# Kernel optimization log

Measured on AMD Instinct MI355X. Metric: run time of the kernel, lower is better.

The kernel has to match this reference:

```python
import jax, jax.numpy as jnp
import numpy as np

D_MODEL = 1024
HEADS = 16
D_K = D_MODEL // HEADS

def setup_inputs() -> dict:
    key = jax.random.key(0)
    ks = jax.random.split(key, 12)
    B, S = 4, 2048
    sc = 1.0 / np.sqrt(D_MODEL)
    inp = {
        'q': jax.random.normal(ks[0], (B, S, D_MODEL), jnp.float32),
        'k': jax.random.normal(ks[1], (B, S, D_MODEL), jnp.float32),
        'v': jax.random.normal(ks[2], (B, S, D_MODEL), jnp.float32),
        'mask': jnp.ones((B, S, S), jnp.int32),
        'Wq': jax.random.normal(ks[3], (D_MODEL, D_MODEL), jnp.float32) * sc,
        'bq': jnp.zeros((D_MODEL,), jnp.float32),
        'Wk': jax.random.normal(ks[4], (D_MODEL, D_MODEL), jnp.float32) * sc,
        'bk': jnp.zeros((D_MODEL,), jnp.float32),
        'Wv': jax.random.normal(ks[5], (D_MODEL, D_MODEL), jnp.float32) * sc,
        'bv': jnp.zeros((D_MODEL,), jnp.float32),
        'Wo': jax.random.normal(ks[6], (D_MODEL, D_MODEL), jnp.float32) * sc,
        'bo': jnp.zeros((D_MODEL,), jnp.float32),
    }
    return inp

def _proj_heads(x, W, b):
    # torch Linear: y = x @ W.T + b; then view(B,S,h,dk).transpose(1,2) -> [B,h,S,dk]
    B, S, _ = x.shape
    y = jnp.einsum('bsd,ed->bse', x, W) + b
    return y.reshape(B, S, HEADS, D_K).transpose(0, 2, 1, 3)

def reference(q, k, v, mask, Wq, bq, Wk, bk, Wv, bv, Wo, bo):
    B, S, _ = q.shape
    qh = _proj_heads(q, Wq, bq)  # [B,h,S,dk]
    kh = _proj_heads(k, Wk, bk)
    vh = _proj_heads(v, Wv, bv)
    scores = jnp.einsum('bhqd,bhkd->bhqk', qh, kh) / np.sqrt(D_K)
    scores = jnp.where(mask[:, None, :, :] == 0, jnp.float32(-1e9), scores)
    probs = jax.nn.softmax(scores, axis=-1)  # dropout = identity (eval mode)
    ctx = jnp.einsum('bhqk,bhkd->bhqd', probs, vh)
    concat = ctx.transpose(0, 2, 1, 3).reshape(B, S, D_MODEL)
    return jnp.einsum('bsd,ed->bse', concat, Wo) + bo
```

## Files before the change

kernel.cpp:

```cpp
#include <hip/hip_runtime.h>
#include <stdint.h>

#define DM 1024
#define SQL 2048
#define NB 4
#define NH 16
#define DK 64

typedef unsigned short u16;
typedef unsigned int u32;
typedef float f32x4 __attribute__((ext_vector_type(4)));
typedef short s16x8 __attribute__((ext_vector_type(8)));
typedef unsigned int u32x2 __attribute__((ext_vector_type(2)));

__device__ __forceinline__ u16 f2bf(float x) {
  union { float f; u32 u; } un; un.f = x;
  return (u16)((un.u + 0x8000u) >> 16);
}
__device__ __forceinline__ u32 pack_bf16(float a, float b) {
  union { float f; u32 u; } ua, ub; ua.f = a; ub.f = b;
  return ((ua.u + 0x8000u) >> 16) | ((ub.u + 0x8000u) & 0xFFFF0000u);
}

typedef __attribute__((address_space(3))) u32 lds_u32_t;
typedef __attribute__((address_space(1))) u32 g_u32_t;

__device__ __forceinline__ void async_cp16(void* lds, const void* g) {
  __builtin_amdgcn_global_load_lds((g_u32_t*)(unsigned long long)g,
                                   (lds_u32_t*)(unsigned long long)lds,
                                   16, 0, 0);
}

__device__ __forceinline__ void mfma16(f32x4& c, s16x8 a, s16x8 b) {
  c = __builtin_amdgcn_mfma_f32_16x16x32_bf16(a, b, c, 0, 0, 0);
}

__device__ __forceinline__ void xcd_tile_map(int flat, int& m0, int& n0) {
  const int xcd = flat & 7;
  const int j = flat >> 3;
  const int p = j >> 5;
  const int dm = (j >> 3) & 3;
  const int nn = j & 7;
  m0 = (p * 32 + xcd * 4 + dm) * 128;
  n0 = nn * 128;
}

__global__ void init_flag_k(int* flag) { if (threadIdx.x == 0) *flag = 1; }

__device__ __forceinline__ void store_bf4(u16* dst, float4 v) {
  u32 lo = pack_bf16(v.x, v.y);
  u32 hi = pack_bf16(v.z, v.w);
  ((u32*)dst)[0] = lo; ((u32*)dst)[1] = hi;
}

__global__ void __launch_bounds__(256) convert_scan_k(
    const float* __restrict__ q, const float* __restrict__ k, const float* __restrict__ v,
    const float* __restrict__ wq, const float* __restrict__ wk,
    const float* __restrict__ wv, const float* __restrict__ wo,
    const int* __restrict__ mask,
    u16* qb, u16* kb, u16* vb, u16* wqb, u16* wkb, u16* wvb, u16* wob, int* flag)
{
  const size_t i = (size_t)blockIdx.x * 256 + threadIdx.x;
  const size_t i4 = i * 4;
  store_bf4(qb + i4, *(const float4*)(q + i4));
  store_bf4(kb + i4, *(const float4*)(k + i4));
  store_bf4(vb + i4, *(const float4*)(v + i4));
  if (i4 < 1048576) {
    store_bf4(wqb + i4, *(const float4*)(wq + i4));
    store_bf4(wkb + i4, *(const float4*)(wk + i4));
    store_bf4(wvb + i4, *(const float4*)(wv + i4));
    store_bf4(wob + i4, *(const float4*)(wo + i4));
  }
  const size_t mi = i * 8;
  int4 m0 = *(const int4*)(mask + mi);
  int4 m1 = *(const int4*)(mask + mi + 4);
  bool z = (m0.x == 0) | (m0.y == 0) | (m0.z == 0) | (m0.w == 0) |
           (m1.x == 0) | (m1.y == 0) | (m1.z == 0) | (m1.w == 0);
  if (z) *flag = 0;
}

__device__ __forceinline__ void gemm_core(const u16* __restrict__ A, const u16* __restrict__ W,
                                          int m0, int n0, u16* sA, u16* sB, f32x4 (&acc)[4][4])
{
  const int tid = threadIdx.x;
  const int l = tid & 63, w = tid >> 6;
  const int g = l >> 4, ln = l & 15;
  const int wm = w & 1, wn = w >> 1;

  for (int kt = 0; kt < DM; kt += 64) {
#pragma unroll
    for (int i = 0; i < 4; ++i) {
      int s = w * 256 + i * 64 + l;
      int m = s >> 3;
      int kc = (s & 7) ^ (m & 7);
      async_cp16(sA + (size_t)(w * 256 + i * 64) * 8,
                 A + (size_t)(m0 + m) * DM + kt + kc * 8);
    }
#pragma unroll
    for (int i = 0; i < 4; ++i) {
      int s = w * 256 + i * 64 + l;
      int n = s >> 3;
      int kc = (s & 7) ^ (n & 7);
      async_cp16(sB + (size_t)(w * 256 + i * 64) * 8,
                 W + (size_t)(n0 + n) * DM + kt + kc * 8);
    }
    asm volatile("s_waitcnt vmcnt(0)" ::: "memory");
    __syncthreads();
#pragma unroll
    for (int ks = 0; ks < 2; ++ks) {
      s16x8 af[4], bfr[4];
#pragma unroll
      for (int mt = 0; mt < 4; ++mt) {
        int m = wm * 64 + mt * 16 + ln;
        int slot = m * 8 + ((ks * 4 + g) ^ (m & 7));
        af[mt] = *(const s16x8*)(sA + (size_t)slot * 8);
      }
#pragma unroll
      for (int nt = 0; nt < 4; ++nt) {
        int n = wn * 64 + nt * 16 + ln;
        int slot = n * 8 + ((ks * 4 + g) ^ (n & 7));
        bfr[nt] = *(const s16x8*)(sB + (size_t)slot * 8);
      }
#pragma unroll
      for (int mt = 0; mt < 4; ++mt)
#pragma unroll
        for (int nt = 0; nt < 4; ++nt)
          mfma16(acc[mt][nt], af[mt], bfr[nt]);
    }
    __syncthreads();
  }
}

__global__ void __launch_bounds__(256) gemm_qkv_k(
    const u16* __restrict__ qb, const u16* __restrict__ kb, const u16* __restrict__ vb,
    const u16* __restrict__ wqb, const u16* __restrict__ wkb, const u16* __restrict__ wvb,
    const float* __restrict__ bq, const float* __restrict__ bk, const float* __restrict__ bv,
    u16* Qh, u16* Kh, u16* Vt)
{
  __shared__ __align__(16) u16 sA[128 * 64];
  __shared__ __align__(16) u16 sB[128 * 64];
  const int z = blockIdx.z;
  const u16* A = (z == 0) ? qb : ((z == 1) ? kb : vb);
  const u16* W = (z == 0) ? wqb : ((z == 1) ? wkb : wvb);
  const float* bias = (z == 0) ? bq : ((z == 1) ? bk : bv);
  int m0, n0;
  xcd_tile_map(blockIdx.x + 8 * blockIdx.y, m0, n0);

  f32x4 zero4 = {0.f, 0.f, 0.f, 0.f};
  f32x4 acc[4][4];
#pragma unroll
  for (int mt = 0; mt < 4; ++mt)
#pragma unroll
    for (int nt = 0; nt < 4; ++nt) acc[mt][nt] = zero4;

  gemm_core(A, W, m0, n0, sA, sB, acc);

  const int tid = threadIdx.x;
  const int l = tid & 63, w = tid >> 6, g = l >> 4, ln = l & 15;
  const int wm = w & 1, wn = w >> 1;
  const float scale = (z == 0) ? (0.125f * 1.44269504089f) : 1.0f;
  u16* Crow = (z == 0) ? Qh : Kh;
#pragma unroll
  for (int nt = 0; nt < 4; ++nt) {
    int n = n0 + wn * 64 + nt * 16 + ln;
    float bn = bias[n];
#pragma unroll
    for (int mt = 0; mt < 4; ++mt) {
      int mb = m0 + wm * 64 + mt * 16 + g * 4;
      f32x4 vv = acc[mt][nt];
      if (z < 2) {
#pragma unroll
        for (int r = 0; r < 4; ++r)
          Crow[(size_t)(mb + r) * DM + n] = f2bf((vv[r] + bn) * scale);
      } else {
        int b = mb >> 11, s = mb & 2047;
        u32 lo = pack_bf16(vv[0] + bn, vv[1] + bn);
        u32 hi = pack_bf16(vv[2] + bn, vv[3] + bn);
        u32* dst = (u32*)(Vt + ((size_t)b << 21) + (size_t)n * SQL + s);
        dst[0] = lo; dst[1] = hi;
      }
    }
  }
}

__device__ __forceinline__ void p_transpose_frag(s16x8& out, u32 x0, u32 x1,
                                                 u32 y0, u32 y1,
                                                 int LA, int LB, bool ghi) {
  union { u32 wds[4]; s16x8 v; } pu;
#if __has_builtin(__builtin_amdgcn_permlane32_swap) && __has_builtin(__builtin_amdgcn_permlane16_swap)
  u32x2 r0 = __builtin_amdgcn_permlane32_swap(x0, y0, false, false);
  u32x2 s0 = __builtin_amdgcn_permlane16_swap(r0.x, r0.y, false, false);
  u32x2 r1 = __builtin_amdgcn_permlane32_swap(x1, y1, false, false);
  u32x2 s1 = __builtin_amdgcn_permlane16_swap(r1.x, r1.y, false, false);
  pu.wds[0] = s0.x; pu.wds[1] = s1.x; pu.wds[2] = s0.y; pu.wds[3] = s1.y;
#else
  u32 a0 = __shfl(x0, LA, 64), a1 = __shfl(x1, LA, 64);
  u32 b0 = __shfl(x0, LB, 64), b1 = __shfl(x1, LB, 64);
  u32 c0 = __shfl(y0, LA, 64), c1 = __shfl(y1, LA, 64);
  u32 d0 = __shfl(y0, LB, 64), d1 = __shfl(y1, LB, 64);
  pu.wds[0] = ghi ? c0 : a0;
  pu.wds[1] = ghi ? c1 : a1;
  pu.wds[2] = ghi ? d0 : b0;
  pu.wds[3] = ghi ? d1 : b1;
#endif
  out = pu.v;
}

__device__ __forceinline__ void attn_tile(
    const u16* Ks, const u16* Vs, int kv0,
    const s16x8 (&qf)[2][2], f32x4 (&ot)[4][2], f32x4 (&sums)[2],
    s16x8 ones, int allones, const int* __restrict__ mask,
    int b, int q0, int w, int g, int ln, int LA, int LB, bool ghi)
{
  f32x4 zero4 = {0.f, 0.f, 0.f, 0.f};
  __builtin_amdgcn_s_setprio(1);
#pragma unroll
  for (int kc = 0; kc < 2; ++kc) {
    f32x4 st[2][2];
#pragma unroll
    for (int t2 = 0; t2 < 2; ++t2)
#pragma unroll
      for (int u = 0; u < 2; ++u) st[t2][u] = zero4;
#pragma unroll
    for (int ks = 0; ks < 2; ++ks) {
#pragma unroll
      for (int t2 = 0; t2 < 2; ++t2) {
        int m = kc * 32 + t2 * 16 + ln;
        int slot = m * 8 + ((ks * 4 + g) ^ (m & 7));
        s16x8 kf = *(const s16x8*)(Ks + (size_t)slot * 8);
#pragma unroll
        for (int u = 0; u < 2; ++u) mfma16(st[t2][u], kf, qf[u][ks]);
      }
    }

    if (!allones) {
      const int* mb_ = mask + (size_t)b * SQL * SQL;
#pragma unroll
      for (int t2 = 0; t2 < 2; ++t2)
#pragma unroll
        for (int u = 0; u < 2; ++u)
#pragma unroll
          for (int r = 0; r < 4; ++r) {
            int kv = kv0 + kc * 32 + t2 * 16 + g * 4 + r;
            int qq = q0 + w * 32 + u * 16 + ln;
            if (mb_[(size_t)qq * SQL + kv] == 0) st[t2][u][r] = -30.f;
          }
    }

    s16x8 pf[2];
#pragma unroll
    for (int u = 0; u < 2; ++u) {
      u32 pkw[2][2];
#pragma unroll
      for (int t2 = 0; t2 < 2; ++t2) {
        float p0 = __builtin_amdgcn_exp2f(st[t2][u][0]);
        float p1 = __builtin_amdgcn_exp2f(st[t2][u][1]);
        float p2 = __builtin_amdgcn_exp2f(st[t2][u][2]);
        float p3 = __builtin_amdgcn_exp2f(st[t2][u][3]);
        pkw[t2][0] = pack_bf16(p0, p1);
        pkw[t2][1] = pack_bf16(p2, p3);
      }
      p_transpose_frag(pf[u], pkw[0][0], pkw[0][1], pkw[1][0], pkw[1][1], LA, LB, ghi);
      mfma16(sums[u], ones, pf[u]);
    }
#pragma unroll
    for (int mt = 0; mt < 4; ++mt) {
      int d = mt * 16 + ln;
      int slot = d * 8 + ((kc * 4 + g) ^ (d & 7));
      s16x8 vf = *(const s16x8*)(Vs + (size_t)slot * 8);
      mfma16(ot[mt][0], vf, pf[0]);
      mfma16(ot[mt][1], vf, pf[1]);
    }
  }
  __builtin_amdgcn_s_setprio(0);
}

__global__ void __launch_bounds__(256, 4) attn_k(
    const u16* __restrict__ Qh, const u16* __restrict__ Kh, const u16* __restrict__ Vt,
    const int* __restrict__ mask, const int* __restrict__ flag, u16* __restrict__ ctx)
{
  __shared__ __align__(16) u16 smem[17408];
  const int tid = threadIdx.x;
  const int l = tid & 63, w = tid >> 6, g = l >> 4, ln = l & 15;
  const int flat = blockIdx.x + 16 * (blockIdx.y + 16 * blockIdx.z);
  const int nid = (flat & 7) * 128 + (flat >> 3);
  const int q0 = (nid & 15) * 128;
  const int bh = nid >> 4;
  const int h = bh & 15, b = bh >> 4;
  const int allones = *flag;

  s16x8 qf[2][2];
#pragma unroll
  for (int u = 0; u < 2; ++u)
#pragma unroll
    for (int ks = 0; ks < 2; ++ks) {
      size_t row = (size_t)(b * SQL + q0 + w * 32 + u * 16 + ln);
      qf[u][ks] = *(const s16x8*)(Qh + row * DM + h * DK + ks * 32 + g * 8);
    }

  f32x4 zero4 = {0.f, 0.f, 0.f, 0.f};
  f32x4 ot[4][2];
#pragma unroll
  for (int mt = 0; mt < 4; ++mt)
#pragma unroll
    for (int u = 0; u < 2; ++u) ot[mt][u] = zero4;
  f32x4 sums[2];
  sums[0] = zero4; sums[1] = zero4;
  s16x8 ones;
#pragma unroll
  for (int i = 0; i < 8; ++i) ones[i] = (short)0x3F80;

  const int LA = (g & 1) * 32 + ln;
  const int LB = LA + 16;
  const bool ghi = (g >> 1) != 0;

  const int s0 = w * 128 + l, s1 = s0 + 64;
  const int m0r = s0 >> 3, m1r = s1 >> 3;
  const int c0 = ((s0 & 7) ^ (m0r & 7)) << 3;
  const int c1 = ((s1 & 7) ^ (m1r & 7)) << 3;
  const u16* gK0 = Kh + (size_t)(b * SQL + m0r) * DM + h * DK + c0;
  const u16* gK1 = Kh + (size_t)(b * SQL + m1r) * DM + h * DK + c1;
  const u16* gV0 = Vt + ((size_t)b << 21) + (size_t)(h * DK + m0r) * SQL + c0;
  const u16* gV1 = Vt + ((size_t)b << 21) + (size_t)(h * DK + m1r) * SQL + c1;
  u16* const dK = smem + (size_t)(w * 128) * 8;

#define STAGE_KV(BUFK, BUFV)                                           \
  do {                                                                 \
    async_cp16(dK + (BUFK), gK0);                                      \
    async_cp16(dK + (BUFK) + 512, gK1);                                \
    async_cp16(dK + (BUFV), gV0);                                      \
    async_cp16(dK + (BUFV) + 512, gV1);                                \
    gK0 += 64 * DM; gK1 += 64 * DM; gV0 += 64; gV1 += 64;              \
  } while (0)

  STAGE_KV(0, 4096);
  __syncthreads();

  for (int t = 0; t < 32; t += 2) {
    STAGE_KV(8192, 12288);
    attn_tile(smem, smem + 4096, t * 64, qf, ot, sums, ones, allones,
              mask, b, q0, w, g, ln, LA, LB, ghi);
    __syncthreads();
    if (t < 30) STAGE_KV(0, 4096);
    attn_tile(smem + 8192, smem + 12288, (t + 1) * 64, qf, ot, sums, ones,
              allones, mask, b, q0, w, g, ln, LA, LB, ghi);
    __syncthreads();
  }
#undef STAGE_KV

  float* red = (float*)smem;
#pragma unroll
  for (int u = 0; u < 2; ++u) {
    float inv = 1.0f / sums[u][0];
    int row = w * 32 + u * 16 + ln;
#pragma unroll
    for (int mt = 0; mt < 4; ++mt) {
      f32x4 vv = ot[mt][u] * inv;
      *(f32x4*)&red[(size_t)row * 68 + mt * 16 + g * 4] = vv;
    }
  }
  __syncthreads();
#pragma unroll
  for (int i = 0; i < 16; ++i) {
    int f2 = i * 256 + tid;
    int qq = f2 >> 5, dp = f2 & 31;
    float2 vv = *(const float2*)&red[(size_t)qq * 68 + dp * 2];
    u32 pkd = pack_bf16(vv.x, vv.y);
    *(u32*)(ctx + (size_t)(b * SQL + q0 + qq) * DM + h * DK + dp * 2) = pkd;
  }
}

__global__ void __launch_bounds__(256) gemm_out_k(
    const u16* __restrict__ ctx, const u16* __restrict__ wob,
    const float* __restrict__ bo, float* __restrict__ out)
{
  __shared__ __align__(16) u16 sA[128 * 64];
  __shared__ __align__(16) u16 sB[128 * 64];
  int m0, n0;
  xcd_tile_map(blockIdx.x + 8 * blockIdx.y, m0, n0);
  f32x4 zero4 = {0.f, 0.f, 0.f, 0.f};
  f32x4 acc[4][4];
#pragma unroll
  for (int mt = 0; mt < 4; ++mt)
#pragma unroll
    for (int nt = 0; nt < 4; ++nt) acc[mt][nt] = zero4;

  gemm_core(ctx, wob, m0, n0, sA, sB, acc);

  const int tid = threadIdx.x;
  const int l = tid & 63, w = tid >> 6, g = l >> 4, ln = l & 15;
  const int wm = w & 1, wn = w >> 1;
#pragma unroll
  for (int nt = 0; nt < 4; ++nt) {
    int n = n0 + wn * 64 + nt * 16 + ln;
    float bn = bo[n];
#pragma unroll
    for (int mt = 0; mt < 4; ++mt) {
      int mb = m0 + wm * 64 + mt * 16 + g * 4;
      f32x4 vv = acc[mt][nt];
#pragma unroll
      for (int r = 0; r < 4; ++r)
        out[(size_t)(mb + r) * DM + n] = vv[r] + bn;
    }
  }
}

extern "C" void kernel_launch(void* const* d_in, const int* in_sizes, int n_in,
                              void* d_out, int out_size, void* d_ws, size_t ws_size,
                              hipStream_t stream) {
  (void)in_sizes; (void)n_in; (void)out_size; (void)ws_size;
  const float* q  = (const float*)d_in[0];
  const float* k  = (const float*)d_in[1];
  const float* v  = (const float*)d_in[2];
  const int* mask = (const int*)d_in[3];
  const float* Wq = (const float*)d_in[4];
  const float* bq = (const float*)d_in[5];
  const float* Wk = (const float*)d_in[6];
  const float* bk = (const float*)d_in[7];
  const float* Wv = (const float*)d_in[8];
  const float* bv = (const float*)d_in[9];
  const float* Wo = (const float*)d_in[10];
  const float* bo = (const float*)d_in[11];
  float* out = (float*)d_out;
  char* ws = (char*)d_ws;

  u16* qb  = (u16*)(ws + 0);
  u16* kb  = (u16*)(ws + 16777216);
  u16* vb  = (u16*)(ws + 33554432);
  u16* Qh  = (u16*)(ws + 50331648);
  u16* Kh  = (u16*)(ws + 67108864);
  u16* Vt  = (u16*)(ws + 83886080);
  u16* ctx = (u16*)(ws + 100663296);
  u16* wqb = (u16*)(ws + 117440512);
  u16* wkb = (u16*)(ws + 119537664);
  u16* wvb = (u16*)(ws + 121634816);
  u16* wob = (u16*)(ws + 123731968);
  int* flag = (int*)(ws + 125829120);

  hipLaunchKernelGGL(init_flag_k, dim3(1), dim3(64), 0, stream, flag);
  hipLaunchKernelGGL(convert_scan_k, dim3(8192), dim3(256), 0, stream,
                     q, k, v, Wq, Wk, Wv, Wo, mask,
                     qb, kb, vb, wqb, wkb, wvb, wob, flag);
  hipLaunchKernelGGL(gemm_qkv_k, dim3(8, 64, 3), dim3(256), 0, stream,
                     qb, kb, vb, wqb, wkb, wvb, bq, bk, bv, Qh, Kh, Vt);
  hipLaunchKernelGGL(attn_k, dim3(16, 16, 4), dim3(256), 0, stream,
                     Qh, Kh, Vt, mask, flag, ctx);
  hipLaunchKernelGGL(gemm_out_k, dim3(8, 64), dim3(256), 0, stream,
                     ctx, wob, bo, out);
}
```

Measured before the change: 378.2 us.

## Shrink attention tiles to 64 queries and 32-key steps for higher occupancy

Each attention block now handles 64 query rows (16 per wave instead of 32), and each loop step stages 32 keys instead of 64. The grid doubles, LDS per block drops to 16 KB, and launch bounds request 8 blocks per CU. The epilogue stages bf16-packed values through LDS with a padded stride instead of fp32. The aim is more resident waves to hide latency, at the cost of loading each K/V tile for twice as many blocks and halving MFMA reuse of each K/V fragment.

```diff
diff --git a/kernel.cpp b/kernel.cpp
--- a/kernel.cpp
+++ b/kernel.cpp
@@ -206,106 +206,88 @@
   out = pu.v;
 }
 
-__device__ __forceinline__ void attn_tile(
+__device__ __forceinline__ void attn_tile32(
     const u16* Ks, const u16* Vs, int kv0,
-    const s16x8 (&qf)[2][2], f32x4 (&ot)[4][2], f32x4 (&sums)[2],
+    const s16x8 (&qf)[2], f32x4 (&ot)[4], f32x4& sums,
     s16x8 ones, int allones, const int* __restrict__ mask,
     int b, int q0, int w, int g, int ln, int LA, int LB, bool ghi)
 {
   f32x4 zero4 = {0.f, 0.f, 0.f, 0.f};
   __builtin_amdgcn_s_setprio(1);
-#pragma unroll
-  for (int kc = 0; kc < 2; ++kc) {
-    f32x4 st[2][2];
+  f32x4 st[2];
+  st[0] = zero4; st[1] = zero4;
+#pragma unroll
+  for (int ks = 0; ks < 2; ++ks) {
+#pragma unroll
+    for (int t2 = 0; t2 < 2; ++t2) {
+      int m = t2 * 16 + ln;
+      int slot = m * 8 + ((ks * 4 + g) ^ (m & 7));
+      s16x8 kf = *(const s16x8*)(Ks + (size_t)slot * 8);
+      mfma16(st[t2], kf, qf[ks]);
+    }
+  }
+
+  if (!allones) {
+    const int* mb_ = mask + (size_t)b * SQL * SQL;
 #pragma unroll
     for (int t2 = 0; t2 < 2; ++t2)
 #pragma unroll
-      for (int u = 0; u < 2; ++u) st[t2][u] = zero4;
-#pragma unroll
-    for (int ks = 0; ks < 2; ++ks) {
-#pragma unroll
-      for (int t2 = 0; t2 < 2; ++t2) {
-        int m = kc * 32 + t2 * 16 + ln;
-        int slot = m * 8 + ((ks * 4 + g) ^ (m & 7));
-        s16x8 kf = *(const s16x8*)(Ks + (size_t)slot * 8);
-#pragma unroll
-        for (int u = 0; u < 2; ++u) mfma16(st[t2][u], kf, qf[u][ks]);
+      for (int r = 0; r < 4; ++r) {
+        int kv = kv0 + t2 * 16 + g * 4 + r;
+        int qq = q0 + w * 16 + ln;
+        if (mb_[(size_t)qq * SQL + kv] == 0) st[t2][r] = -30.f;
       }
-    }
-
-    if (!allones) {
-      const int* mb_ = mask + (size_t)b * SQL * SQL;
-#pragma unroll
-      for (int t2 = 0; t2 < 2; ++t2)
-#pragma unroll
-        for (int u = 0; u < 2; ++u)
-#pragma unroll
-          for (int r = 0; r < 4; ++r) {
-            int kv = kv0 + kc * 32 + t2 * 16 + g * 4 + r;
-            int qq = q0 + w * 32 + u * 16 + ln;
-            if (mb_[(size_t)qq * SQL + kv] == 0) st[t2][u][r] = -30.f;
-          }
-    }
-
-    s16x8 pf[2];
-#pragma unroll
-    for (int u = 0; u < 2; ++u) {
-      u32 pkw[2][2];
-#pragma unroll
-      for (int t2 = 0; t2 < 2; ++t2) {
-        float p0 = __builtin_amdgcn_exp2f(st[t2][u][0]);
-        float p1 = __builtin_amdgcn_exp2f(st[t2][u][1]);
-        float p2 = __builtin_amdgcn_exp2f(st[t2][u][2]);
-        float p3 = __builtin_amdgcn_exp2f(st[t2][u][3]);
-        pkw[t2][0] = pack_bf16(p0, p1);
-        pkw[t2][1] = pack_bf16(p2, p3);
-      }
-      p_transpose_frag(pf[u], pkw[0][0], pkw[0][1], pkw[1][0], pkw[1][1], LA, LB, ghi);
-      mfma16(sums[u], ones, pf[u]);
-    }
-#pragma unroll
-    for (int mt = 0; mt < 4; ++mt) {
-      int d = mt * 16 + ln;
-      int slot = d * 8 + ((kc * 4 + g) ^ (d & 7));
-      s16x8 vf = *(const s16x8*)(Vs + (size_t)slot * 8);
-      mfma16(ot[mt][0], vf, pf[0]);
-      mfma16(ot[mt][1], vf, pf[1]);
-    }
+  }
+
+  u32 pkw[2][2];
+#pragma unroll
+  for (int t2 = 0; t2 < 2; ++t2) {
+    float p0 = __builtin_amdgcn_exp2f(st[t2][0]);
+    float p1 = __builtin_amdgcn_exp2f(st[t2][1]);
+    float p2 = __builtin_amdgcn_exp2f(st[t2][2]);
+    float p3 = __builtin_amdgcn_exp2f(st[t2][3]);
+    pkw[t2][0] = pack_bf16(p0, p1);
+    pkw[t2][1] = pack_bf16(p2, p3);
+  }
+  s16x8 pf;
+  p_transpose_frag(pf, pkw[0][0], pkw[0][1], pkw[1][0], pkw[1][1], LA, LB, ghi);
+  mfma16(sums, ones, pf);
+#pragma unroll
+  for (int mt = 0; mt < 4; ++mt) {
+    int d = mt * 16 + ln;
+    int slot = d * 4 + (g ^ ((d >> 1) & 3));
+    s16x8 vf = *(const s16x8*)(Vs + (size_t)slot * 8);
+    mfma16(ot[mt], vf, pf);
   }
   __builtin_amdgcn_s_setprio(0);
 }
 
-__global__ void __launch_bounds__(256, 4) attn_k(
+__global__ void __launch_bounds__(256, 8) attn_k(
     const u16* __restrict__ Qh, const u16* __restrict__ Kh, const u16* __restrict__ Vt,
     const int* __restrict__ mask, const int* __restrict__ flag, u16* __restrict__ ctx)
 {
-  __shared__ __align__(16) u16 smem[17408];
+  __shared__ __align__(16) u16 smem[8192];
   const int tid = threadIdx.x;
   const int l = tid & 63, w = tid >> 6, g = l >> 4, ln = l & 15;
-  const int flat = blockIdx.x + 16 * (blockIdx.y + 16 * blockIdx.z);
-  const int nid = (flat & 7) * 128 + (flat >> 3);
-  const int q0 = (nid & 15) * 128;
-  const int bh = nid >> 4;
+  const int flat = blockIdx.x + 32 * (blockIdx.y + 16 * blockIdx.z);
+  const int nid = (flat & 7) * 256 + (flat >> 3);
+  const int q0 = (nid & 31) * 64;
+  const int bh = nid >> 5;
   const int h = bh & 15, b = bh >> 4;
   const int allones = *flag;
 
-  s16x8 qf[2][2];
-#pragma unroll
-  for (int u = 0; u < 2; ++u)
-#pragma unroll
-    for (int ks = 0; ks < 2; ++ks) {
-      size_t row = (size_t)(b * SQL + q0 + w * 32 + u * 16 + ln);
-      qf[u][ks] = *(const s16x8*)(Qh + row * DM + h * DK + ks * 32 + g * 8);
-    }
+  s16x8 qf[2];
+#pragma unroll
+  for (int ks = 0; ks < 2; ++ks) {
+    size_t row = (size_t)(b * SQL + q0 + w * 16 + ln);
+    qf[ks] = *(const s16x8*)(Qh + row * DM + h * DK + ks * 32 + g * 8);
+  }
 
   f32x4 zero4 = {0.f, 0.f, 0.f, 0.f};
-  f32x4 ot[4][2];
-#pragma unroll
-  for (int mt = 0; mt < 4; ++mt)
-#pragma unroll
-    for (int u = 0; u < 2; ++u) ot[mt][u] = zero4;
-  f32x4 sums[2];
-  sums[0] = zero4; sums[1] = zero4;
+  f32x4 ot[4];
+#pragma unroll
+  for (int mt = 0; mt < 4; ++mt) ot[mt] = zero4;
+  f32x4 sums = zero4;
   s16x8 ones;
 #pragma unroll
   for (int i = 0; i < 8; ++i) ones[i] = (short)0x3F80;
@@ -314,59 +296,55 @@
   const int LB = LA + 16;
   const bool ghi = (g >> 1) != 0;
 
-  const int s0 = w * 128 + l, s1 = s0 + 64;
-  const int m0r = s0 >> 3, m1r = s1 >> 3;
-  const int c0 = ((s0 & 7) ^ (m0r & 7)) << 3;
-  const int c1 = ((s1 & 7) ^ (m1r & 7)) << 3;
-  const u16* gK0 = Kh + (size_t)(b * SQL + m0r) * DM + h * DK + c0;
-  const u16* gK1 = Kh + (size_t)(b * SQL + m1r) * DM + h * DK + c1;
-  const u16* gV0 = Vt + ((size_t)b << 21) + (size_t)(h * DK + m0r) * SQL + c0;
-  const u16* gV1 = Vt + ((size_t)b << 21) + (size_t)(h * DK + m1r) * SQL + c1;
-  u16* const dK = smem + (size_t)(w * 128) * 8;
+  const int mK = tid >> 3;
+  const int cK = ((tid & 7) ^ (mK & 7)) << 3;
+  const u16* gK = Kh + (size_t)(b * SQL + mK) * DM + h * DK + cK;
+  const int dV = tid >> 2;
+  const int cV = ((tid & 3) ^ ((dV >> 1) & 3)) << 3;
+  const u16* gV = Vt + ((size_t)b << 21) + (size_t)(h * DK + dV) * SQL + cV;
+  u16* const dst = smem + (size_t)w * 512;
 
 #define STAGE_KV(BUFK, BUFV)                                           \
   do {                                                                 \
-    async_cp16(dK + (BUFK), gK0);                                      \
-    async_cp16(dK + (BUFK) + 512, gK1);                                \
-    async_cp16(dK + (BUFV), gV0);                                      \
-    async_cp16(dK + (BUFV) + 512, gV1);                                \
-    gK0 += 64 * DM; gK1 += 64 * DM; gV0 += 64; gV1 += 64;              \
+    async_cp16(dst + (BUFK), gK);                                      \
+    async_cp16(dst + (BUFV), gV);                                      \
+    gK += 32 * DM; gV += 32;                                           \
   } while (0)
 
-  STAGE_KV(0, 4096);
+  STAGE_KV(0, 2048);
   __syncthreads();
 
-  for (int t = 0; t < 32; t += 2) {
-    STAGE_KV(8192, 12288);
-    attn_tile(smem, smem + 4096, t * 64, qf, ot, sums, ones, allones,
-              mask, b, q0, w, g, ln, LA, LB, ghi);
+  for (int t = 0; t < 64; t += 2) {
+    STAGE_KV(4096, 6144);
+    attn_tile32(smem, smem + 2048, t * 32, qf, ot, sums, ones, allones,
+                mask, b, q0, w, g, ln, LA, LB, ghi);
     __syncthreads();
-    if (t < 30) STAGE_KV(0, 4096);
-    attn_tile(smem + 8192, smem + 12288, (t + 1) * 64, qf, ot, sums, ones,
-              allones, mask, b, q0, w, g, ln, LA, LB, ghi);
+    if (t < 62) STAGE_KV(0, 2048);
+    attn_tile32(smem + 4096, smem + 6144, (t + 1) * 32, qf, ot, sums, ones,
+                allones, mask, b, q0, w, g, ln, LA, LB, ghi);
     __syncthreads();
   }
 #undef STAGE_KV
 
-  float* red = (float*)smem;
-#pragma unroll
-  for (int u = 0; u < 2; ++u) {
-    float inv = 1.0f / sums[u][0];
-    int row = w * 32 + u * 16 + ln;
+  u32* red = (u32*)smem;
+  {
+    float inv = 1.0f / sums[0];
+    int row = w * 16 + ln;
 #pragma unroll
     for (int mt = 0; mt < 4; ++mt) {
-      f32x4 vv = ot[mt][u] * inv;
-      *(f32x4*)&red[(size_t)row * 68 + mt * 16 + g * 4] = vv;
+      f32x4 vv = ot[mt] * inv;
+      int col = mt * 8 + g * 2;
+      red[(size_t)row * 33 + col]     = pack_bf16(vv[0], vv[1]);
+      red[(size_t)row * 33 + col + 1] = pack_bf16(vv[2], vv[3]);
     }
   }
   __syncthreads();
 #pragma unroll
-  for (int i = 0; i < 16; ++i) {
+  for (int i = 0; i < 8; ++i) {
     int f2 = i * 256 + tid;
     int qq = f2 >> 5, dp = f2 & 31;
-    float2 vv = *(const float2*)&red[(size_t)qq * 68 + dp * 2];
-    u32 pkd = pack_bf16(vv.x, vv.y);
-    *(u32*)(ctx + (size_t)(b * SQL + q0 + qq) * DM + h * DK + dp * 2) = pkd;
+    *(u32*)(ctx + (size_t)(b * SQL + q0 + qq) * DM + h * DK + dp * 2) =
+        red[(size_t)qq * 33 + dp];
   }
 }
 
@@ -443,7 +421,7 @@
                      qb, kb, vb, wqb, wkb, wvb, wob, flag);
   hipLaunchKernelGGL(gemm_qkv_k, dim3(8, 64, 3), dim3(256), 0, stream,
                      qb, kb, vb, wqb, wkb, wvb, bq, bk, bv, Qh, Kh, Vt);
-  hipLaunchKernelGGL(attn_k, dim3(16, 16, 4), dim3(256), 0, stream,
+  hipLaunchKernelGGL(attn_k, dim3(32, 16, 4), dim3(256), 0, stream,
                      Qh, Kh, Vt, mask, flag, ctx);
   hipLaunchKernelGGL(gemm_out_k, dim3(8, 64), dim3(256), 0, stream,
                      ctx, wob, bo, out);
```

After: 400.8 us. 1.06x slower.

## Double-buffer LDS tiles in projection GEMMs to overlap loads with MFMA

Applied to the files above, without the earlier changes.

Splits the GEMM main loop into separate stage (async global-to-LDS copy) and compute helpers. The next K-tile now loads into a second LDS buffer while the current tile is computed, aiming to hide global memory latency behind the MFMA work in the QKV and output projection kernels. It removes the explicit vmcnt wait and relies on the barrier to order the async copies. LDS use per block doubles, which may lower occupancy.

```diff
diff --git a/kernel.cpp b/kernel.cpp
--- a/kernel.cpp
+++ b/kernel.cpp
@@ -79,54 +79,73 @@
   if (z) *flag = 0;
 }
 
-__device__ __forceinline__ void gemm_core(const u16* __restrict__ A, const u16* __restrict__ W,
-                                          int m0, int n0, u16* sA, u16* sB, f32x4 (&acc)[4][4])
+__device__ __forceinline__ void gemm_stage(const u16* __restrict__ A,
+                                           const u16* __restrict__ W,
+                                           int m0, int n0, int kt,
+                                           u16* sA, u16* sB, int w, int l) {
+#pragma unroll
+  for (int i = 0; i < 4; ++i) {
+    int s = w * 256 + i * 64 + l;
+    int m = s >> 3;
+    int kc = (s & 7) ^ (m & 7);
+    async_cp16(sA + (size_t)(w * 256 + i * 64) * 8,
+               A + (size_t)(m0 + m) * DM + kt + kc * 8);
+  }
+#pragma unroll
+  for (int i = 0; i < 4; ++i) {
+    int s = w * 256 + i * 64 + l;
+    int n = s >> 3;
+    int kc = (s & 7) ^ (n & 7);
+    async_cp16(sB + (size_t)(w * 256 + i * 64) * 8,
+               W + (size_t)(n0 + n) * DM + kt + kc * 8);
+  }
+}
+
+__device__ __forceinline__ void gemm_compute(const u16* sA, const u16* sB,
+                                             f32x4 (&acc)[4][4],
+                                             int wm, int wn, int g, int ln) {
+#pragma unroll
+  for (int ks = 0; ks < 2; ++ks) {
+    s16x8 af[4], bfr[4];
+#pragma unroll
+    for (int mt = 0; mt < 4; ++mt) {
+      int m = wm * 64 + mt * 16 + ln;
+      int slot = m * 8 + ((ks * 4 + g) ^ (m & 7));
+      af[mt] = *(const s16x8*)(sA + (size_t)slot * 8);
+    }
+#pragma unroll
+    for (int nt = 0; nt < 4; ++nt) {
+      int n = wn * 64 + nt * 16 + ln;
+      int slot = n * 8 + ((ks * 4 + g) ^ (n & 7));
+      bfr[nt] = *(const s16x8*)(sB + (size_t)slot * 8);
+    }
+#pragma unroll
+    for (int mt = 0; mt < 4; ++mt)
+#pragma unroll
+      for (int nt = 0; nt < 4; ++nt)
+        mfma16(acc[mt][nt], af[mt], bfr[nt]);
+  }
+}
+
+__device__ __forceinline__ void gemm_core(const u16* __restrict__ A,
+                                          const u16* __restrict__ W,
+                                          int m0, int n0,
+                                          u16* sA0, u16* sB0, u16* sA1, u16* sB1,
+                                          f32x4 (&acc)[4][4])
 {
   const int tid = threadIdx.x;
   const int l = tid & 63, w = tid >> 6;
   const int g = l >> 4, ln = l & 15;
   const int wm = w & 1, wn = w >> 1;
 
-  for (int kt = 0; kt < DM; kt += 64) {
-#pragma unroll
-    for (int i = 0; i < 4; ++i) {
-      int s = w * 256 + i * 64 + l;
-      int m = s >> 3;
-      int kc = (s & 7) ^ (m & 7);
-      async_cp16(sA + (size_t)(w * 256 + i * 64) * 8,
-                 A + (size_t)(m0 + m) * DM + kt + kc * 8);
-    }
-#pragma unroll
-    for (int i = 0; i < 4; ++i) {
-      int s = w * 256 + i * 64 + l;
-      int n = s >> 3;
-      int kc = (s & 7) ^ (n & 7);
-      async_cp16(sB + (size_t)(w * 256 + i * 64) * 8,
-                 W + (size_t)(n0 + n) * DM + kt + kc * 8);
-    }
-    asm volatile("s_waitcnt vmcnt(0)" ::: "memory");
+  gemm_stage(A, W, m0, n0, 0, sA0, sB0, w, l);
+  __syncthreads();
+  for (int kt = 0; kt < DM; kt += 128) {
+    gemm_stage(A, W, m0, n0, kt + 64, sA1, sB1, w, l);
+    gemm_compute(sA0, sB0, acc, wm, wn, g, ln);
     __syncthreads();
-#pragma unroll
-    for (int ks = 0; ks < 2; ++ks) {
-      s16x8 af[4], bfr[4];
-#pragma unroll
-      for (int mt = 0; mt < 4; ++mt) {
-        int m = wm * 64 + mt * 16 + ln;
-        int slot = m * 8 + ((ks * 4 + g) ^ (m & 7));
-        af[mt] = *(const s16x8*)(sA + (size_t)slot * 8);
-      }
-#pragma unroll
-      for (int nt = 0; nt < 4; ++nt) {
-        int n = wn * 64 + nt * 16 + ln;
-        int slot = n * 8 + ((ks * 4 + g) ^ (n & 7));
-        bfr[nt] = *(const s16x8*)(sB + (size_t)slot * 8);
-      }
-#pragma unroll
-      for (int mt = 0; mt < 4; ++mt)
-#pragma unroll
-        for (int nt = 0; nt < 4; ++nt)
-          mfma16(acc[mt][nt], af[mt], bfr[nt]);
-    }
+    if (kt + 128 < DM) gemm_stage(A, W, m0, n0, kt + 128, sA0, sB0, w, l);
+    gemm_compute(sA1, sB1, acc, wm, wn, g, ln);
     __syncthreads();
   }
 }
@@ -137,8 +156,8 @@
     const float* __restrict__ bq, const float* __restrict__ bk, const float* __restrict__ bv,
     u16* Qh, u16* Kh, u16* Vt)
 {
-  __shared__ __align__(16) u16 sA[128 * 64];
-  __shared__ __align__(16) u16 sB[128 * 64];
+  __shared__ __align__(16) u16 sA[2][128 * 64];
+  __shared__ __align__(16) u16 sB[2][128 * 64];
   const int z = blockIdx.z;
   const u16* A = (z == 0) ? qb : ((z == 1) ? kb : vb);
   const u16* W = (z == 0) ? wqb : ((z == 1) ? wkb : wvb);
@@ -153,7 +172,7 @@
 #pragma unroll
     for (int nt = 0; nt < 4; ++nt) acc[mt][nt] = zero4;
 
-  gemm_core(A, W, m0, n0, sA, sB, acc);
+  gemm_core(A, W, m0, n0, sA[0], sB[0], sA[1], sB[1], acc);
 
   const int tid = threadIdx.x;
   const int l = tid & 63, w = tid >> 6, g = l >> 4, ln = l & 15;
@@ -374,8 +393,8 @@
     const u16* __restrict__ ctx, const u16* __restrict__ wob,
     const float* __restrict__ bo, float* __restrict__ out)
 {
-  __shared__ __align__(16) u16 sA[128 * 64];
-  __shared__ __align__(16) u16 sB[128 * 64];
+  __shared__ __align__(16) u16 sA[2][128 * 64];
+  __shared__ __align__(16) u16 sB[2][128 * 64];
   int m0, n0;
   xcd_tile_map(blockIdx.x + 8 * blockIdx.y, m0, n0);
   f32x4 zero4 = {0.f, 0.f, 0.f, 0.f};
@@ -385,7 +404,7 @@
 #pragma unroll
     for (int nt = 0; nt < 4; ++nt) acc[mt][nt] = zero4;
 
-  gemm_core(ctx, wob, m0, n0, sA, sB, acc);
+  gemm_core(ctx, wob, m0, n0, sA[0], sB[0], sA[1], sB[1], acc);
 
   const int tid = threadIdx.x;
   const int l = tid & 63, w = tid >> 6, g = l >> 4, ln = l & 15;
```

Result: no change. 380.7 us (+0.7%).
